# Kernel tuning notes

Hardware: AMD Instinct MI355X
Metric: run time of the kernel (lower is better)

The kernel has to match this reference:

```python
import jax, jax.numpy as jnp
import numpy as np
import math

EPS_RMS = 1.1920929e-07  # torch nn.RMSNorm default eps = finfo(float32).eps
EPS_DEN = 1e-6


def rmsnorm(x, gamma):
    ms = jnp.mean(x * x, axis=-1, keepdims=True)
    return x * jax.lax.rsqrt(ms + EPS_RMS) * gamma


def setup_inputs() -> dict:
    key = jax.random.key(0)
    ks = jax.random.split(key, 8)
    B, T, K, D = 4, 4096, 256, 1024
    x_tokens = jax.random.normal(ks[0], (B, T, D), dtype=jnp.float32)
    ctx = jax.random.normal(ks[1], (B, K, D), dtype=jnp.float32)
    idx = jnp.sort(jax.random.randint(ks[2], (B, T), 0, K), axis=-1)
    s = 1.0 / math.sqrt(D)
    Wq = jax.random.normal(ks[3], (D, D), dtype=jnp.float32) * s
    Wk = jax.random.normal(ks[4], (D, D), dtype=jnp.float32) * s
    Wv = jax.random.normal(ks[5], (D, D), dtype=jnp.float32) * s
    Wo = jax.random.normal(ks[6], (D, D), dtype=jnp.float32) * s
    return {
        'x_tokens': x_tokens, 'ctx': ctx, 'ctx_index_per_token': idx,
        'gamma_q': jnp.ones((D,), jnp.float32), 'gamma_kv': jnp.ones((D,), jnp.float32),
        'Wq': Wq, 'Wk': Wk, 'Wv': Wv, 'Wo': Wo,
    }


def reference(x_tokens, ctx, ctx_index_per_token, gamma_q, gamma_kv, Wq, Wk, Wv, Wo):
    B, T, D = x_tokens.shape
    K = ctx.shape[1]
    H = 16
    hd = D // H

    def split(x):  # (B,S,D) -> (B,H,S,hd)
        return x.reshape(B, -1, H, hd).transpose(0, 2, 1, 3)

    q = split(rmsnorm(x_tokens, gamma_q) @ Wq.T)
    kn = rmsnorm(ctx, gamma_kv)
    k = split(kn @ Wk.T)
    v = split(kn @ Wv.T)

    # band mask: |ctx_pos - idx| <= 1, shape (B,1,T,K)
    ctx_pos = jnp.arange(K)[None, None, :]
    mask = (jnp.abs(ctx_pos - ctx_index_per_token[:, :, None]) <= 1)[:, None]

    scores = jnp.einsum('bhqd,bhkd->bhqk', q, k) / math.sqrt(hd)
    w = jnp.square(jax.nn.relu(scores))
    w = jnp.where(mask, w, 0.0)
    denom = jnp.maximum(w.sum(-1, keepdims=True), EPS_DEN)
    out = jnp.einsum('bhqk,bhkd->bhqd', w / denom, v)
    out = out.transpose(0, 2, 1, 3).reshape(B, T, D)
    return x_tokens + out @ Wo.T
```

## Files before the change

kernel.cpp:

```cpp
#include <hip/hip_runtime.h>
#include <hip/hip_bf16.h>
#include <stdint.h>

#define D_DIM 1024

using f32x4  = __attribute__((ext_vector_type(4))) float;
using short8 = __attribute__((ext_vector_type(8))) short;

__device__ __forceinline__ float bf2f(unsigned short u) {
    union { unsigned int i; float f; } v; v.i = ((unsigned int)u) << 16; return v.f;
}
__device__ __forceinline__ unsigned short f2bf(float f) {
    union { float f; unsigned int i; } v; v.f = f;
    unsigned int x = v.i;
    return (unsigned short)((x + 0x7fffu + ((x >> 16) & 1u)) >> 16);
}
__device__ __forceinline__ void gload16(const void* g, void* l) {
    __builtin_amdgcn_global_load_lds(
        (const __attribute__((address_space(1))) void*)g,
        (__attribute__((address_space(3))) void*)l, 16, 0, 0);
}

__global__ __launch_bounds__(256)
void convw_kernel(const float* __restrict__ Wk, const float* __restrict__ Wv,
                  const float* __restrict__ Wo, const float* __restrict__ gkv,
                  unsigned short* __restrict__ wk_hi, unsigned short* __restrict__ wk_lo,
                  unsigned short* __restrict__ wv_hi, unsigned short* __restrict__ wv_lo,
                  unsigned short* __restrict__ wo_b)
{
    const int e   = (blockIdx.x * 256 + threadIdx.x) * 4;
    const int sel = e >> 20;
    const int off = e & 0xFFFFF;
    const float* src = sel == 0 ? Wk : sel == 1 ? Wv : Wo;
    float4 v = *(const float4*)(src + off);
    if (sel < 2) {
        float4 g = *(const float4*)(gkv + (off & 1023));
        v.x *= g.x; v.y *= g.y; v.z *= g.z; v.w *= g.w;
        ushort4 h, l;
        h.x = f2bf(v.x); l.x = f2bf(v.x - bf2f(h.x));
        h.y = f2bf(v.y); l.y = f2bf(v.y - bf2f(h.y));
        h.z = f2bf(v.z); l.z = f2bf(v.z - bf2f(h.z));
        h.w = f2bf(v.w); l.w = f2bf(v.w - bf2f(h.w));
        unsigned short* hi = sel == 0 ? wk_hi : wv_hi;
        unsigned short* lo = sel == 0 ? wk_lo : wv_lo;
        *(ushort4*)(hi + off) = h;
        *(ushort4*)(lo + off) = l;
    } else {
        ushort4 o;
        o.x = f2bf(v.x); o.y = f2bf(v.y); o.z = f2bf(v.z); o.w = f2bf(v.w);
        *(ushort4*)(wo_b + off) = o;
    }
}

__global__ __launch_bounds__(256)
void transq_kernel(const float* __restrict__ Wq, const float* __restrict__ gq,
                   unsigned short* __restrict__ th, unsigned short* __restrict__ tl)
{
    __shared__ float tile[64][65];
    const int c0 = (blockIdx.x & 15) * 64;
    const int i0 = (blockIdx.x >> 4) * 64;
    const int tid = threadIdx.x;
#pragma unroll
    for (int j = 0; j < 4; ++j) {
        const int e  = tid + j * 256;
        const int rl = e >> 4;
        const int q4 = e & 15;
        float4 v = *(const float4*)(Wq + (long)(c0 + rl) * 1024 + i0 + q4 * 4);
        tile[q4 * 4 + 0][rl] = v.x;
        tile[q4 * 4 + 1][rl] = v.y;
        tile[q4 * 4 + 2][rl] = v.z;
        tile[q4 * 4 + 3][rl] = v.w;
    }
    __syncthreads();
#pragma unroll
    for (int j = 0; j < 4; ++j) {
        const int e  = tid + j * 256;
        const int il = e >> 4;
        const int s4 = e & 15;
        const float g = gq[i0 + il];
        float v0 = tile[il][s4 * 4 + 0] * g;
        float v1 = tile[il][s4 * 4 + 1] * g;
        float v2 = tile[il][s4 * 4 + 2] * g;
        float v3 = tile[il][s4 * 4 + 3] * g;
        ushort4 hh, ll;
        hh.x = f2bf(v0); ll.x = f2bf(v0 - bf2f(hh.x));
        hh.y = f2bf(v1); ll.y = f2bf(v1 - bf2f(hh.y));
        hh.z = f2bf(v2); ll.z = f2bf(v2 - bf2f(hh.z));
        hh.w = f2bf(v3); ll.w = f2bf(v3 - bf2f(hh.w));
        const long o = (long)(i0 + il) * 1024 + c0 + s4 * 4;
        *(ushort4*)(th + o) = hh;
        *(ushort4*)(tl + o) = ll;
    }
}

__global__ __launch_bounds__(256)
void rms_split_kernel(const float* __restrict__ x,
                      unsigned short* __restrict__ xh, unsigned short* __restrict__ xl)
{
    const long row = blockIdx.x;
    float4 v = ((const float4*)(x + row * D_DIM))[threadIdx.x];
    float ss = v.x*v.x + v.y*v.y + v.z*v.z + v.w*v.w;
#pragma unroll
    for (int m = 32; m; m >>= 1) ss += __shfl_xor(ss, m);
    __shared__ float red[4];
    if ((threadIdx.x & 63) == 0) red[threadIdx.x >> 6] = ss;
    __syncthreads();
    const float tot = red[0] + red[1] + red[2] + red[3];
    const float scale = rsqrtf(tot * (1.0f / 1024.0f) + 1.1920929e-07f);
    v.x *= scale; v.y *= scale; v.z *= scale; v.w *= scale;
    ushort4 h, l;
    h.x = f2bf(v.x); l.x = f2bf(v.x - bf2f(h.x));
    h.y = f2bf(v.y); l.y = f2bf(v.y - bf2f(h.y));
    h.z = f2bf(v.z); l.z = f2bf(v.z - bf2f(h.z));
    h.w = f2bf(v.w); l.w = f2bf(v.w - bf2f(h.w));
    *(ushort4*)(xh + row * D_DIM + threadIdx.x * 4) = h;
    *(ushort4*)(xl + row * D_DIM + threadIdx.x * 4) = l;
}

__global__ __launch_bounds__(256)
void gemm_kv(const unsigned short* __restrict__ ch, const unsigned short* __restrict__ cl,
             const unsigned short* __restrict__ wkh, const unsigned short* __restrict__ wkl,
             const unsigned short* __restrict__ wvh,
             unsigned short* __restrict__ kh, unsigned short* __restrict__ kl,
             float* __restrict__ v_f)
{
    __shared__ unsigned short Ah[4096], Al[4096], Bh[4096], Bl[4096];
    const bool full = (blockIdx.z == 0);
    const unsigned short* Bhp = full ? wkh : wvh;
    const unsigned short* Blp = wkl;

    const int tid = threadIdx.x, lane = tid & 63, wave = tid >> 6;
    const int wm = wave >> 1, wn = wave & 1;
    const long Arow0 = (long)blockIdx.y * 128;
    const int  Brow0 = blockIdx.x * 128;
    const int fr = lane & 15, ks = lane >> 4;
    const int ksz = (ks ^ ((fr >> 1) & 3)) << 4;
    const int kq  = ((tid & 3) ^ ((tid >> 3) & 3)) * 8;
    const int srow = tid >> 2;

    const long a_off0 = (Arow0 + srow) * D_DIM + kq;
    const long a_off1 = (Arow0 + srow + 64) * D_DIM + kq;
    const long b_off0 = (long)(Brow0 + srow) * D_DIM + kq;
    const long b_off1 = (long)(Brow0 + srow + 64) * D_DIM + kq;

    f32x4 acc[4][4] = {};
    char* AhB = (char*)Ah; char* AlB = (char*)Al;
    char* BhB = (char*)Bh; char* BlB = (char*)Bl;

    for (int kt = 0; kt < 32; ++kt) {
        const int k0 = kt * 32;
        gload16(ch + a_off0 + k0, AhB + tid * 16);
        gload16(ch + a_off1 + k0, AhB + 4096 + tid * 16);
        gload16(Bhp + b_off0 + k0, BhB + tid * 16);
        gload16(Bhp + b_off1 + k0, BhB + 4096 + tid * 16);
        if (full) {
            gload16(cl + a_off0 + k0, AlB + tid * 16);
            gload16(cl + a_off1 + k0, AlB + 4096 + tid * 16);
            gload16(Blp + b_off0 + k0, BlB + tid * 16);
            gload16(Blp + b_off1 + k0, BlB + 4096 + tid * 16);
        }
        __syncthreads();

        short8 ah[4], al[4], bh[4], bl[4];
#pragma unroll
        for (int mi = 0; mi < 4; ++mi) {
            const int aoff = (wm * 64 + mi * 16 + fr) * 64 + ksz;
            ah[mi] = *(const short8*)(AhB + aoff);
            if (full) al[mi] = *(const short8*)(AlB + aoff);
        }
#pragma unroll
        for (int ni = 0; ni < 4; ++ni) {
            const int boff = (wn * 64 + ni * 16 + fr) * 64 + ksz;
            bh[ni] = *(const short8*)(BhB + boff);
            if (full) bl[ni] = *(const short8*)(BlB + boff);
        }
#pragma unroll
        for (int mi = 0; mi < 4; ++mi)
#pragma unroll
            for (int ni = 0; ni < 4; ++ni) {
                acc[mi][ni] = __builtin_amdgcn_mfma_f32_16x16x32_bf16(ah[mi], bh[ni], acc[mi][ni], 0, 0, 0);
                if (full) {
                    acc[mi][ni] = __builtin_amdgcn_mfma_f32_16x16x32_bf16(al[mi], bh[ni], acc[mi][ni], 0, 0, 0);
                    acc[mi][ni] = __builtin_amdgcn_mfma_f32_16x16x32_bf16(ah[mi], bl[ni], acc[mi][ni], 0, 0, 0);
                }
            }
        __syncthreads();
    }

    const int c = lane & 15, r0 = (lane >> 4) * 4;
#pragma unroll
    for (int mi = 0; mi < 4; ++mi)
#pragma unroll
        for (int ni = 0; ni < 4; ++ni)
#pragma unroll
            for (int j = 0; j < 4; ++j) {
                const long row = Arow0 + wm * 64 + mi * 16 + r0 + j;
                const int  col = Brow0 + wn * 64 + ni * 16 + c;
                const float val = acc[mi][ni][j];
                if (full) {
                    const unsigned short hh = f2bf(val);
                    kh[row * D_DIM + col] = hh;
                    kl[row * D_DIM + col] = f2bf(val - bf2f(hh));
                } else {
                    v_f[row * D_DIM + col] = val;
                }
            }
}

__global__ __launch_bounds__(256)
void gemm_U(const unsigned short* __restrict__ kh, const unsigned short* __restrict__ kl,
            const unsigned short* __restrict__ th, const unsigned short* __restrict__ tl,
            unsigned short* __restrict__ Uh, unsigned short* __restrict__ Ul)
{
    __shared__ unsigned short Ah[4096], Al[4096], Bh[4096], Bl[4096];
    const int h = blockIdx.z;
    const int tid = threadIdx.x, lane = tid & 63, wave = tid >> 6;
    const int wm = wave >> 1, wn = wave & 1;
    const long Arow0 = (long)blockIdx.y * 128;
    const int  Brow0 = blockIdx.x * 128;
    const int fr = lane & 15, ks = lane >> 4;
    const int ksz = (ks ^ ((fr >> 1) & 3)) << 4;
    const int kq  = ((tid & 3) ^ ((tid >> 3) & 3)) * 8;
    const int srow = tid >> 2;
    const int kb = h * 64;

    const long a_off0 = (Arow0 + srow) * D_DIM + kb + kq;
    const long a_off1 = (Arow0 + srow + 64) * D_DIM + kb + kq;
    const long b_off0 = (long)(Brow0 + srow) * D_DIM + kb + kq;
    const long b_off1 = (long)(Brow0 + srow + 64) * D_DIM + kb + kq;

    f32x4 acc[4][4] = {};
    char* AhB = (char*)Ah; char* AlB = (char*)Al;
    char* BhB = (char*)Bh; char* BlB = (char*)Bl;

    for (int kt = 0; kt < 2; ++kt) {
        const int k0 = kt * 32;
        gload16(kh + a_off0 + k0, AhB + tid * 16);
        gload16(kh + a_off1 + k0, AhB + 4096 + tid * 16);
        gload16(kl + a_off0 + k0, AlB + tid * 16);
        gload16(kl + a_off1 + k0, AlB + 4096 + tid * 16);
        gload16(th + b_off0 + k0, BhB + tid * 16);
        gload16(th + b_off1 + k0, BhB + 4096 + tid * 16);
        gload16(tl + b_off0 + k0, BlB + tid * 16);
        gload16(tl + b_off1 + k0, BlB + 4096 + tid * 16);
        __syncthreads();

        short8 ah[4], al[4], bh[4], bl[4];
#pragma unroll
        for (int mi = 0; mi < 4; ++mi) {
            const int aoff = (wm * 64 + mi * 16 + fr) * 64 + ksz;
            ah[mi] = *(const short8*)(AhB + aoff);
            al[mi] = *(const short8*)(AlB + aoff);
        }
#pragma unroll
        for (int ni = 0; ni < 4; ++ni) {
            const int boff = (wn * 64 + ni * 16 + fr) * 64 + ksz;
            bh[ni] = *(const short8*)(BhB + boff);
            bl[ni] = *(const short8*)(BlB + boff);
        }
#pragma unroll
        for (int mi = 0; mi < 4; ++mi)
#pragma unroll
            for (int ni = 0; ni < 4; ++ni) {
                acc[mi][ni] = __builtin_amdgcn_mfma_f32_16x16x32_bf16(ah[mi], bh[ni], acc[mi][ni], 0, 0, 0);
                acc[mi][ni] = __builtin_amdgcn_mfma_f32_16x16x32_bf16(al[mi], bh[ni], acc[mi][ni], 0, 0, 0);
                acc[mi][ni] = __builtin_amdgcn_mfma_f32_16x16x32_bf16(ah[mi], bl[ni], acc[mi][ni], 0, 0, 0);
            }
        __syncthreads();
    }

    const int c = lane & 15, r0 = (lane >> 4) * 4;
#pragma unroll
    for (int mi = 0; mi < 4; ++mi)
#pragma unroll
        for (int ni = 0; ni < 4; ++ni)
#pragma unroll
            for (int j = 0; j < 4; ++j) {
                const long row = Arow0 + wm * 64 + mi * 16 + r0 + j;
                const int  col = Brow0 + wn * 64 + ni * 16 + c;
                const float val = acc[mi][ni][j];
                const long o = ((long)row * 16 + h) * 1024 + col;
                const unsigned short hh = f2bf(val);
                Uh[o] = hh;
                Ul[o] = f2bf(val - bf2f(hh));
            }
}

__global__ __launch_bounds__(256)
void score_gemm(const float* __restrict__ x, const int* __restrict__ cidx,
                const unsigned short* __restrict__ Uh, const unsigned short* __restrict__ Ul,
                float* __restrict__ sbuf, float* __restrict__ ssbuf)
{
    const int pg = blockIdx.x;
    const int mh = blockIdx.y;
    const int bz = blockIdx.z;
    const int b  = bz & 3;
    const int ksp = bz >> 2;
    const int kbase = ksp << 9;
    const int p0 = pg * 4;
    const int* ci = cidx + (b << 12);
    int l = 0, r = 4096;
    while (l < r) { int m = (l + r) >> 1; if (ci[m] < p0 - 1) l = m + 1; else r = m; }
    const int lo = l;
    r = 4096;
    while (l < r) { int m = (l + r) >> 1; if (ci[m] <= p0 + 4) l = m + 1; else r = m; }
    const int hi = l;
    if (lo + mh * 64 >= hi) return;

    float* const sb = sbuf + (long)ksp * 786432;
    float* const ssb = ssbuf + (ksp << 14);

    __shared__ unsigned short AhS[2][2048], AlS[2][2048];
    __shared__ unsigned short UhS[2][2048], UlS[2][2048];

    const int tid = threadIdx.x, lane = tid & 63, wave = tid >> 6;
    const int fr = lane & 15;
    const int ks = lane >> 4;
    const int ksz = (ks ^ ((fr >> 1) & 3)) << 4;

    const int arow = tid >> 2, aq = tid & 3;
    const int aslot = aq ^ ((arow >> 1) & 3);
    const unsigned short* const Uhb = Uh + ((long)((b << 8) + p0) * 16) * 1024 + kbase;
    const unsigned short* const Ulb = Ul + ((long)((b << 8) + p0) * 16) * 1024 + kbase;
    const float* const xb = x + ((long)b << 12) * 1024 + kbase;

    for (int t0 = lo + mh * 64; t0 < hi; t0 += 128) {
        const int tc0 = (t0 + arow < hi) ? (t0 + arow) : (hi - 1);
        const float* xr = xb + (long)tc0 * 1024 + aq * 8;
        float ss = 0.f;

        gload16(Uhb + (long)arow * 1024 + aslot * 8, (char*)&UhS[0][0] + tid * 16);
        gload16(Ulb + (long)arow * 1024 + aslot * 8, (char*)&UlS[0][0] + tid * 16);
        {
            const float4 v0 = *(const float4*)(xr);
            const float4 v1 = *(const float4*)(xr + 4);
            ss += v0.x*v0.x + v0.y*v0.y + v0.z*v0.z + v0.w*v0.w
                + v1.x*v1.x + v1.y*v1.y + v1.z*v1.z + v1.w*v1.w;
            short8 hv, lv;
            unsigned short h_;
            h_ = f2bf(v0.x); hv[0] = (short)h_; lv[0] = (short)f2bf(v0.x - bf2f(h_));
            h_ = f2bf(v0.y); hv[1] = (short)h_; lv[1] = (short)f2bf(v0.y - bf2f(h_));
            h_ = f2bf(v0.z); hv[2] = (short)h_; lv[2] = (short)f2bf(v0.z - bf2f(h_));
            h_ = f2bf(v0.w); hv[3] = (short)h_; lv[3] = (short)f2bf(v0.w - bf2f(h_));
            h_ = f2bf(v1.x); hv[4] = (short)h_; lv[4] = (short)f2bf(v1.x - bf2f(h_));
            h_ = f2bf(v1.y); hv[5] = (short)h_; lv[5] = (short)f2bf(v1.y - bf2f(h_));
            h_ = f2bf(v1.z); hv[6] = (short)h_; lv[6] = (short)f2bf(v1.z - bf2f(h_));
            h_ = f2bf(v1.w); hv[7] = (short)h_; lv[7] = (short)f2bf(v1.w - bf2f(h_));
            *(short8*)((char*)&AhS[0][0] + arow * 64 + aslot * 16) = hv;
            *(short8*)((char*)&AlS[0][0] + arow * 64 + aslot * 16) = lv;
        }
        __syncthreads();

        f32x4 acc[4] = {};
        for (int t = 0; t < 16; ++t) {
            const int cur = t & 1, nxt = cur ^ 1;
            float4 v0, v1;
            if (t < 15) {
                const int k0n = (t + 1) * 32;
                gload16(Uhb + (long)arow * 1024 + k0n + aslot * 8, (char*)&UhS[nxt][0] + tid * 16);
                gload16(Ulb + (long)arow * 1024 + k0n + aslot * 8, (char*)&UlS[nxt][0] + tid * 16);
                v0 = *(const float4*)(xr + k0n);
                v1 = *(const float4*)(xr + k0n + 4);
            }

            const int aoff = cur * 4096 + (wave * 16 + fr) * 64 + ksz;
            const short8 ah = *(const short8*)((char*)&AhS[0][0] + aoff);
            const short8 al = *(const short8*)((char*)&AlS[0][0] + aoff);
#pragma unroll
            for (int ni = 0; ni < 4; ++ni) {
                const int boff = cur * 4096 + (ni * 16 + fr) * 64 + ksz;
                const short8 uh = *(const short8*)((char*)&UhS[0][0] + boff);
                const short8 ul = *(const short8*)((char*)&UlS[0][0] + boff);
                acc[ni] = __builtin_amdgcn_mfma_f32_16x16x32_bf16(ah, uh, acc[ni], 0, 0, 0);
                acc[ni] = __builtin_amdgcn_mfma_f32_16x16x32_bf16(al, uh, acc[ni], 0, 0, 0);
                acc[ni] = __builtin_amdgcn_mfma_f32_16x16x32_bf16(ah, ul, acc[ni], 0, 0, 0);
            }

            if (t < 15) {
                ss += v0.x*v0.x + v0.y*v0.y + v0.z*v0.z + v0.w*v0.w
                    + v1.x*v1.x + v1.y*v1.y + v1.z*v1.z + v1.w*v1.w;
                short8 hv, lv;
                unsigned short h_;
                h_ = f2bf(v0.x); hv[0] = (short)h_; lv[0] = (short)f2bf(v0.x - bf2f(h_));
                h_ = f2bf(v0.y); hv[1] = (short)h_; lv[1] = (short)f2bf(v0.y - bf2f(h_));
                h_ = f2bf(v0.z); hv[2] = (short)h_; lv[2] = (short)f2bf(v0.z - bf2f(h_));
                h_ = f2bf(v0.w); hv[3] = (short)h_; lv[3] = (short)f2bf(v0.w - bf2f(h_));
                h_ = f2bf(v1.x); hv[4] = (short)h_; lv[4] = (short)f2bf(v1.x - bf2f(h_));
                h_ = f2bf(v1.y); hv[5] = (short)h_; lv[5] = (short)f2bf(v1.y - bf2f(h_));
                h_ = f2bf(v1.z); hv[6] = (short)h_; lv[6] = (short)f2bf(v1.z - bf2f(h_));
                h_ = f2bf(v1.w); hv[7] = (short)h_; lv[7] = (short)f2bf(v1.w - bf2f(h_));
                *(short8*)((char*)&AhS[0][0] + nxt * 4096 + arow * 64 + aslot * 16) = hv;
                *(short8*)((char*)&AlS[0][0] + nxt * 4096 + arow * 64 + aslot * 16) = lv;
            }
            __syncthreads();
        }

        ss += __shfl_xor(ss, 1);
        ss += __shfl_xor(ss, 2);
        if (aq == 0 && t0 + arow < hi)
            ssb[(b << 12) + t0 + arow] = ss;

        const int hcol = lane & 15;
        const int r0j = (lane >> 4) * 4;
#pragma unroll
        for (int j = 0; j < 4; ++j) {
            const int trow = t0 + wave * 16 + r0j + j;
            if (trow < hi) {
                const long tg = ((long)b << 12) + trow;
                const int idx = ci[trow];
#pragma unroll
                for (int ni = 0; ni < 4; ++ni) {
                    const int dp = p0 + ni - idx + 1;
                    if (dp >= 0 && dp <= 2)
                        sb[(tg * 16 + hcol) * 3 + dp] = acc[ni][j];
                }
            }
        }
        __syncthreads();
    }
}

__global__ __launch_bounds__(256)
void attnout_kernel(const float* __restrict__ sbuf, const float* __restrict__ ssbuf,
                    const float* __restrict__ vf, const int* __restrict__ cidx,
                    unsigned short* __restrict__ ao)
{
    const int tid = threadIdx.x;
    const int tg = tid >> 4, h = tid & 15;
    const int t = blockIdx.x * 16 + tg;
    const int b = t >> 12;
    const int idx = cidx[t];
    const float* sb0 = sbuf + ((long)t * 16 + h) * 3;
    const float* sb1 = sb0 + 786432;
    const float ssum = ssbuf[t] + ssbuf[t + 16384];
    const float scale = rsqrtf(ssum * (1.0f / 1024.0f) + 1.1920929e-07f) * 0.125f;
    float w0 = 0.f, w1 = 0.f, w2 = 0.f, wsum = 0.f;
    if (idx - 1 >= 0) { float s = (sb0[0] + sb1[0]) * scale; if (s > 0.f) { w0 = s * s; wsum += w0; } }
    { float s = (sb0[1] + sb1[1]) * scale; if (s > 0.f) { w1 = s * s; wsum += w1; } }
    if (idx + 1 < 256) { float s = (sb0[2] + sb1[2]) * scale; if (s > 0.f) { w2 = s * s; wsum += w2; } }
    const float inv = 1.0f / fmaxf(wsum, 1e-6f);
    w0 *= inv; w1 *= inv; w2 *= inv;
    const int p0 = idx > 0 ? idx - 1 : 0;
    const int p2 = idx < 255 ? idx + 1 : 255;
    const float4* v0 = (const float4*)(vf + ((long)(b * 256 + p0)) * 1024 + h * 64);
    const float4* v1 = (const float4*)(vf + ((long)(b * 256 + idx)) * 1024 + h * 64);
    const float4* v2 = (const float4*)(vf + ((long)(b * 256 + p2)) * 1024 + h * 64);
    ushort4* aop = (ushort4*)(ao + (long)t * 1024 + h * 64);
#pragma unroll
    for (int q = 0; q < 16; ++q) {
        float4 a0 = v0[q], a1 = v1[q], a2 = v2[q];
        ushort4 o;
        o.x = f2bf(w0 * a0.x + w1 * a1.x + w2 * a2.x);
        o.y = f2bf(w0 * a0.y + w1 * a1.y + w2 * a2.y);
        o.z = f2bf(w0 * a0.z + w1 * a1.z + w2 * a2.z);
        o.w = f2bf(w0 * a0.w + w1 * a1.w + w2 * a2.w);
        aop[q] = o;
    }
}

__global__ __launch_bounds__(512, 2)
void gemm_out256(const unsigned short* __restrict__ A,
                 const unsigned short* __restrict__ W,
                 float* __restrict__ C, const float* __restrict__ resid)
{
    __shared__ unsigned short As[4][8192];
    __shared__ unsigned short Bs[4][8192];

    const int lin = blockIdx.x;
    const int bx = (lin >> 3) & 3;
    const int by = ((lin >> 5) << 3) | (lin & 7);
    const long row0 = (long)by * 256;
    const int  col0 = bx * 256;

    const int tid = threadIdx.x, lane = tid & 63, wave = tid >> 6;
    const int wm = wave >> 2, wn = wave & 3;
    const int fr = lane & 15, ks = lane >> 4;
    const int ksz = (ks ^ ((fr >> 1) & 3)) << 4;
    const int kq  = ((tid & 3) ^ ((tid >> 3) & 3)) * 8;
    const int srow = tid >> 2;

    const long a_off0 = (row0 + srow) * D_DIM + kq;
    const long a_off1 = (row0 + 128 + srow) * D_DIM + kq;
    const long b_off0 = (long)(col0 + srow) * D_DIM + kq;
    const long b_off1 = (long)(col0 + 128 + srow) * D_DIM + kq;

    f32x4 acc[8][4] = {};

#define STAGE_A(X) do { const int kofs_ = (X) * 32;                          \
    char* base_ = (char*)&As[(X) & 3][0];                                    \
    gload16(A + a_off0 + kofs_, base_ + tid * 16);                           \
    gload16(A + a_off1 + kofs_, base_ + 8192 + tid * 16); } while (0)
#define STAGE_B(X) do { const int kofs_ = (X) * 32;                          \
    char* base_ = (char*)&Bs[(X) & 3][0];                                    \
    gload16(W + b_off0 + kofs_, base_ + tid * 16);                           \
    gload16(W + b_off1 + kofs_, base_ + 8192 + tid * 16); } while (0)

    STAGE_A(0); STAGE_B(0); STAGE_A(1); STAGE_B(1); STAGE_A(2); STAGE_B(2);
    asm volatile("s_waitcnt vmcnt(4)" ::: "memory");
    __builtin_amdgcn_s_barrier();
    __builtin_amdgcn_sched_barrier(0);

    short8 bfrag[4];

    for (int i = 0; i < 8; ++i) {
        const int Tb = i * 4;
        const bool last = (i == 7);
#pragma unroll
        for (int ph = 0; ph < 8; ++ph) {
            const int tp = ph >> 1;
            const int h  = ph & 1;
            const int rg = tp;
            if (h == 0) {
#pragma unroll
                for (int ni = 0; ni < 4; ++ni)
                    bfrag[ni] = *(const short8*)((char*)&Bs[rg][0] +
                                (wn * 64 + ni * 16 + fr) * 64 + ksz);
            }
            short8 afrag[4];
#pragma unroll
            for (int mi = 0; mi < 4; ++mi)
                afrag[mi] = *(const short8*)((char*)&As[rg][0] +
                            (wm * 128 + h * 64 + mi * 16 + fr) * 64 + ksz);
            {
                const int SX = Tb + 3 + tp;
                if (SX < 32) {
                    if (h == 0) STAGE_A(SX); else STAGE_B(SX);
                }
            }
            if (ph == 3) {
                if (last) asm volatile("s_waitcnt vmcnt(0)" ::: "memory");
                else      asm volatile("s_waitcnt vmcnt(4)" ::: "memory");
            } else if (ph == 7) {
                if (!last) asm volatile("s_waitcnt vmcnt(4)" ::: "memory");
            }
            __builtin_amdgcn_s_barrier();
            asm volatile("s_waitcnt lgkmcnt(0)" ::: "memory");
            __builtin_amdgcn_sched_barrier(0);
            __builtin_amdgcn_s_setprio(1);
#pragma unroll
            for (int mi = 0; mi < 4; ++mi)
#pragma unroll
                for (int ni = 0; ni < 4; ++ni)
                    acc[h * 4 + mi][ni] = __builtin_amdgcn_mfma_f32_16x16x32_bf16(
                        afrag[mi], bfrag[ni], acc[h * 4 + mi][ni], 0, 0, 0);
            __builtin_amdgcn_s_setprio(0);
            __builtin_amdgcn_sched_barrier(0);
            __builtin_amdgcn_s_barrier();
            __builtin_amdgcn_sched_barrier(0);
        }
    }
#undef STAGE_A
#undef STAGE_B

    const int c = lane & 15, rg2 = lane >> 4;
#pragma unroll
    for (int mi = 0; mi < 8; ++mi)
#pragma unroll
        for (int ni = 0; ni < 4; ++ni)
#pragma unroll
            for (int j = 0; j < 4; ++j) {
                const long row = row0 + wm * 128 + mi * 16 + rg2 * 4 + j;
                const int  col = col0 + wn * 64 + ni * 16 + c;
                C[row * D_DIM + col] = resid[row * D_DIM + col] + acc[mi][ni][j];
            }
}

extern "C" void kernel_launch(void* const* d_in, const int* in_sizes, int n_in,
                              void* d_out, int out_size, void* d_ws, size_t ws_size,
                              hipStream_t stream)
{
    const float* x    = (const float*)d_in[0];
    const float* ctx  = (const float*)d_in[1];
    const int*   cidx = (const int*)d_in[2];
    const float* gq   = (const float*)d_in[3];
    const float* gkv  = (const float*)d_in[4];
    const float* Wq   = (const float*)d_in[5];
    const float* Wk   = (const float*)d_in[6];
    const float* Wv   = (const float*)d_in[7];
    const float* Wo   = (const float*)d_in[8];
    float* out = (float*)d_out;

    char* ws = (char*)d_ws;
    const size_t MB = 1 << 20;
    unsigned short* wqT_hi = (unsigned short*)(ws + 0 * MB);
    unsigned short* wqT_lo = (unsigned short*)(ws + 2 * MB);
    unsigned short* wk_hi  = (unsigned short*)(ws + 4 * MB);
    unsigned short* wk_lo  = (unsigned short*)(ws + 6 * MB);
    unsigned short* wv_hi  = (unsigned short*)(ws + 8 * MB);
    unsigned short* wv_lo  = (unsigned short*)(ws + 10 * MB);
    unsigned short* wo_b   = (unsigned short*)(ws + 12 * MB);
    unsigned short* ch = (unsigned short*)(ws + 14 * MB);
    unsigned short* cl = (unsigned short*)(ws + 16 * MB);
    unsigned short* kh = (unsigned short*)(ws + 18 * MB);
    unsigned short* kl = (unsigned short*)(ws + 20 * MB);
    float* v_f = (float*)(ws + 22 * MB);
    unsigned short* Uh = (unsigned short*)(ws + 26 * MB);
    unsigned short* Ul = (unsigned short*)(ws + 58 * MB);
    unsigned short* ao_b = (unsigned short*)(ws + 26 * MB);
    float* sbuf  = (float*)(ws + 91 * MB);
    float* ssbuf = (float*)(ws + 97 * MB);

    convw_kernel<<<3072, 256, 0, stream>>>(Wk, Wv, Wo, gkv,
                                           wk_hi, wk_lo, wv_hi, wv_lo, wo_b);
    transq_kernel<<<256, 256, 0, stream>>>(Wq, gq, wqT_hi, wqT_lo);
    rms_split_kernel<<<1024, 256, 0, stream>>>(ctx, ch, cl);
    gemm_kv<<<dim3(8, 8, 2), 256, 0, stream>>>(ch, cl, wk_hi, wk_lo, wv_hi,
                                               kh, kl, v_f);
    gemm_U<<<dim3(8, 8, 16), 256, 0, stream>>>(kh, kl, wqT_hi, wqT_lo, Uh, Ul);
    score_gemm<<<dim3(64, 2, 8), 256, 0, stream>>>(x, cidx, Uh, Ul, sbuf, ssbuf);
    attnout_kernel<<<1024, 256, 0, stream>>>(sbuf, ssbuf, v_f, cidx, ao_b);
    gemm_out256<<<256, 512, 0, stream>>>(ao_b, wo_b, out, x);
}
```

Before: 191.8 us.

## Deepen score-kernel pipeline to 4-stage U buffers with manual waitcnt and priority

```diff
diff --git a/kernel.cpp b/kernel.cpp
--- a/kernel.cpp
+++ b/kernel.cpp
@@ -311,7 +311,7 @@
     float* const ssb = ssbuf + (ksp << 14);
 
     __shared__ unsigned short AhS[2][2048], AlS[2][2048];
-    __shared__ unsigned short UhS[2][2048], UlS[2][2048];
+    __shared__ unsigned short UhS[4][2048], UlS[4][2048];
 
     const int tid = threadIdx.x, lane = tid & 63, wave = tid >> 6;
     const int fr = lane & 15;
@@ -324,75 +324,81 @@
     const unsigned short* const Ulb = Ul + ((long)((b << 8) + p0) * 16) * 1024 + kbase;
     const float* const xb = x + ((long)b << 12) * 1024 + kbase;
 
+#define USTAGE(T) do {                                                        \
+    const int kofs_ = (T) * 32;                                               \
+    gload16(Uhb + (long)arow * 1024 + kofs_ + aslot * 8,                      \
+            (char*)&UhS[(T) & 3][0] + tid * 16);                              \
+    gload16(Ulb + (long)arow * 1024 + kofs_ + aslot * 8,                      \
+            (char*)&UlS[(T) & 3][0] + tid * 16); } while (0)
+
+#define SPLITW(RG, V0, V1) do {                                               \
+    ss += V0.x*V0.x + V0.y*V0.y + V0.z*V0.z + V0.w*V0.w                       \
+        + V1.x*V1.x + V1.y*V1.y + V1.z*V1.z + V1.w*V1.w;                      \
+    short8 hv, lv; unsigned short h_;                                         \
+    h_ = f2bf(V0.x); hv[0] = (short)h_; lv[0] = (short)f2bf(V0.x - bf2f(h_)); \
+    h_ = f2bf(V0.y); hv[1] = (short)h_; lv[1] = (short)f2bf(V0.y - bf2f(h_)); \
+    h_ = f2bf(V0.z); hv[2] = (short)h_; lv[2] = (short)f2bf(V0.z - bf2f(h_)); \
+    h_ = f2bf(V0.w); hv[3] = (short)h_; lv[3] = (short)f2bf(V0.w - bf2f(h_)); \
+    h_ = f2bf(V1.x); hv[4] = (short)h_; lv[4] = (short)f2bf(V1.x - bf2f(h_)); \
+    h_ = f2bf(V1.y); hv[5] = (short)h_; lv[5] = (short)f2bf(V1.y - bf2f(h_)); \
+    h_ = f2bf(V1.z); hv[6] = (short)h_; lv[6] = (short)f2bf(V1.z - bf2f(h_)); \
+    h_ = f2bf(V1.w); hv[7] = (short)h_; lv[7] = (short)f2bf(V1.w - bf2f(h_)); \
+    *(short8*)((char*)&AhS[RG][0] + arow * 64 + aslot * 16) = hv;             \
+    *(short8*)((char*)&AlS[RG][0] + arow * 64 + aslot * 16) = lv; } while (0)
+
+#define ITER(T, XC0, XC1, XN0, XN1) do {                                      \
+    if ((T) + 2 <= 15) {                                                      \
+        const float* xp_ = xr + ((T) + 2) * 32;                               \
+        XN0 = *(const float4*)(xp_); XN1 = *(const float4*)(xp_ + 4);         \
+    }                                                                         \
+    if ((T) + 3 <= 15) USTAGE((T) + 3);                                       \
+    {                                                                         \
+        const int aoff_ = (((T) & 1)) * 4096 + (wave * 16 + fr) * 64 + ksz;   \
+        const short8 ah_ = *(const short8*)((char*)&AhS[0][0] + aoff_);       \
+        const short8 al_ = *(const short8*)((char*)&AlS[0][0] + aoff_);       \
+        __builtin_amdgcn_s_setprio(1);                                        \
+        _Pragma("unroll")                                                     \
+        for (int ni = 0; ni < 4; ++ni) {                                      \
+            const int boff_ = (((T) & 3)) * 4096 + (ni * 16 + fr) * 64 + ksz; \
+            const short8 uh_ = *(const short8*)((char*)&UhS[0][0] + boff_);   \
+            const short8 ul_ = *(const short8*)((char*)&UlS[0][0] + boff_);   \
+            acc[ni] = __builtin_amdgcn_mfma_f32_16x16x32_bf16(ah_, uh_, acc[ni], 0, 0, 0); \
+            acc[ni] = __builtin_amdgcn_mfma_f32_16x16x32_bf16(al_, uh_, acc[ni], 0, 0, 0); \
+            acc[ni] = __builtin_amdgcn_mfma_f32_16x16x32_bf16(ah_, ul_, acc[ni], 0, 0, 0); \
+        }                                                                     \
+        __builtin_amdgcn_s_setprio(0);                                        \
+    }                                                                         \
+    if ((T) >= 12) asm volatile("s_waitcnt vmcnt(0)" ::: "memory");           \
+    else           asm volatile("s_waitcnt vmcnt(6)" ::: "memory");           \
+    __builtin_amdgcn_sched_barrier(0);                                        \
+    if ((T) + 1 <= 15) SPLITW(((T) + 1) & 1, XC0, XC1);                       \
+    asm volatile("s_waitcnt lgkmcnt(0)" ::: "memory");                        \
+    __builtin_amdgcn_sched_barrier(0);                                        \
+    __builtin_amdgcn_s_barrier();                                             \
+    __builtin_amdgcn_sched_barrier(0); } while (0)
+
     for (int t0 = lo + mh * 64; t0 < hi; t0 += 128) {
         const int tc0 = (t0 + arow < hi) ? (t0 + arow) : (hi - 1);
         const float* xr = xb + (long)tc0 * 1024 + aq * 8;
         float ss = 0.f;
 
-        gload16(Uhb + (long)arow * 1024 + aslot * 8, (char*)&UhS[0][0] + tid * 16);
-        gload16(Ulb + (long)arow * 1024 + aslot * 8, (char*)&UlS[0][0] + tid * 16);
-        {
-            const float4 v0 = *(const float4*)(xr);
-            const float4 v1 = *(const float4*)(xr + 4);
-            ss += v0.x*v0.x + v0.y*v0.y + v0.z*v0.z + v0.w*v0.w
-                + v1.x*v1.x + v1.y*v1.y + v1.z*v1.z + v1.w*v1.w;
-            short8 hv, lv;
-            unsigned short h_;
-            h_ = f2bf(v0.x); hv[0] = (short)h_; lv[0] = (short)f2bf(v0.x - bf2f(h_));
-            h_ = f2bf(v0.y); hv[1] = (short)h_; lv[1] = (short)f2bf(v0.y - bf2f(h_));
-            h_ = f2bf(v0.z); hv[2] = (short)h_; lv[2] = (short)f2bf(v0.z - bf2f(h_));
-            h_ = f2bf(v0.w); hv[3] = (short)h_; lv[3] = (short)f2bf(v0.w - bf2f(h_));
-            h_ = f2bf(v1.x); hv[4] = (short)h_; lv[4] = (short)f2bf(v1.x - bf2f(h_));
-            h_ = f2bf(v1.y); hv[5] = (short)h_; lv[5] = (short)f2bf(v1.y - bf2f(h_));
-            h_ = f2bf(v1.z); hv[6] = (short)h_; lv[6] = (short)f2bf(v1.z - bf2f(h_));
-            h_ = f2bf(v1.w); hv[7] = (short)h_; lv[7] = (short)f2bf(v1.w - bf2f(h_));
-            *(short8*)((char*)&AhS[0][0] + arow * 64 + aslot * 16) = hv;
-            *(short8*)((char*)&AlS[0][0] + arow * 64 + aslot * 16) = lv;
-        }
-        __syncthreads();
+        float4 xa0, xa1, xb0, xb1;
+        xa0 = *(const float4*)(xr); xa1 = *(const float4*)(xr + 4);
+        USTAGE(0); USTAGE(1);
+        xb0 = *(const float4*)(xr + 32); xb1 = *(const float4*)(xr + 36);
+        USTAGE(2);
+        SPLITW(0, xa0, xa1);
+        asm volatile("s_waitcnt vmcnt(4)" ::: "memory");
+        asm volatile("s_waitcnt lgkmcnt(0)" ::: "memory");
+        __builtin_amdgcn_sched_barrier(0);
+        __builtin_amdgcn_s_barrier();
+        __builtin_amdgcn_sched_barrier(0);
 
         f32x4 acc[4] = {};
-        for (int t = 0; t < 16; ++t) {
-            const int cur = t & 1, nxt = cur ^ 1;
-            float4 v0, v1;
-            if (t < 15) {
-                const int k0n = (t + 1) * 32;
-                gload16(Uhb + (long)arow * 1024 + k0n + aslot * 8, (char*)&UhS[nxt][0] + tid * 16);
-                gload16(Ulb + (long)arow * 1024 + k0n + aslot * 8, (char*)&UlS[nxt][0] + tid * 16);
-                v0 = *(const float4*)(xr + k0n);
-                v1 = *(const float4*)(xr + k0n + 4);
-            }
-
-            const int aoff = cur * 4096 + (wave * 16 + fr) * 64 + ksz;
-            const short8 ah = *(const short8*)((char*)&AhS[0][0] + aoff);
-            const short8 al = *(const short8*)((char*)&AlS[0][0] + aoff);
-#pragma unroll
-            for (int ni = 0; ni < 4; ++ni) {
-                const int boff = cur * 4096 + (ni * 16 + fr) * 64 + ksz;
-                const short8 uh = *(const short8*)((char*)&UhS[0][0] + boff);
-                const short8 ul = *(const short8*)((char*)&UlS[0][0] + boff);
-                acc[ni] = __builtin_amdgcn_mfma_f32_16x16x32_bf16(ah, uh, acc[ni], 0, 0, 0);
-                acc[ni] = __builtin_amdgcn_mfma_f32_16x16x32_bf16(al, uh, acc[ni], 0, 0, 0);
-                acc[ni] = __builtin_amdgcn_mfma_f32_16x16x32_bf16(ah, ul, acc[ni], 0, 0, 0);
-            }
-
-            if (t < 15) {
-                ss += v0.x*v0.x + v0.y*v0.y + v0.z*v0.z + v0.w*v0.w
-                    + v1.x*v1.x + v1.y*v1.y + v1.z*v1.z + v1.w*v1.w;
-                short8 hv, lv;
-                unsigned short h_;
-                h_ = f2bf(v0.x); hv[0] = (short)h_; lv[0] = (short)f2bf(v0.x - bf2f(h_));
-                h_ = f2bf(v0.y); hv[1] = (short)h_; lv[1] = (short)f2bf(v0.y - bf2f(h_));
-                h_ = f2bf(v0.z); hv[2] = (short)h_; lv[2] = (short)f2bf(v0.z - bf2f(h_));
-                h_ = f2bf(v0.w); hv[3] = (short)h_; lv[3] = (short)f2bf(v0.w - bf2f(h_));
-                h_ = f2bf(v1.x); hv[4] = (short)h_; lv[4] = (short)f2bf(v1.x - bf2f(h_));
-                h_ = f2bf(v1.y); hv[5] = (short)h_; lv[5] = (short)f2bf(v1.y - bf2f(h_));
-                h_ = f2bf(v1.z); hv[6] = (short)h_; lv[6] = (short)f2bf(v1.z - bf2f(h_));
-                h_ = f2bf(v1.w); hv[7] = (short)h_; lv[7] = (short)f2bf(v1.w - bf2f(h_));
-                *(short8*)((char*)&AhS[0][0] + nxt * 4096 + arow * 64 + aslot * 16) = hv;
-                *(short8*)((char*)&AlS[0][0] + nxt * 4096 + arow * 64 + aslot * 16) = lv;
-            }
-            __syncthreads();
+#pragma unroll
+        for (int tt = 0; tt < 16; tt += 2) {
+            ITER(tt,     xb0, xb1, xa0, xa1);
+            ITER(tt + 1, xa0, xa1, xb0, xb1);
         }
 
         ss += __shfl_xor(ss, 1);
@@ -418,6 +424,9 @@
         }
         __syncthreads();
     }
+#undef USTAGE
+#undef SPLITW
+#undef ITER
 }
 
 __global__ __launch_bounds__(256)
```

Measured after the change: 228.1 us. 18.9% more time.
